# Kernel tuning notes

Hardware: AMD Instinct MI355X
Metric: run time of the kernel (lower is better)

The kernel has to match this reference:

```python
import jax, jax.numpy as jnp
import numpy as np

H, P, G, NS, K = 8, 64, 64, 64, 3          # heads, dim_head, slice_num, d_state, d_conv
D_INNER = H * P                            # 512
CONV_DIM = D_INNER + 2 * NS                # 640
D_IN_PROJ = 2 * D_INNER + 2 * NS + 2 * H   # 1168


def setup_inputs() -> dict:
    key = jax.random.key(0)
    ks = jax.random.split(key, 10)
    dim, Bsz, N = 256, 4, 8192
    s = 0.02
    return {
        "x": jax.random.normal(ks[0], (Bsz, N, dim), jnp.float32),
        "W_fx": jax.random.normal(ks[1], (D_INNER, dim), jnp.float32) * s,
        "b_fx": jnp.zeros((D_INNER,), jnp.float32),
        "W_x": jax.random.normal(ks[2], (D_INNER, dim), jnp.float32) * s,
        "b_x": jnp.zeros((D_INNER,), jnp.float32),
        "W_slice": jax.random.normal(ks[3], (G, P), jnp.float32) * s,
        "b_slice": jnp.zeros((G,), jnp.float32),
        "temperature": jnp.full((1, H, 1, 1), 0.5, jnp.float32),
        "hy_in_w": jax.random.normal(ks[4], (D_IN_PROJ, D_INNER), jnp.float32) * s,
        "hy_conv_w": jax.random.normal(ks[5], (CONV_DIM, K), jnp.float32) * s,
        "hy_conv_b": jnp.zeros((CONV_DIM,), jnp.float32),
        "hy_dt_bias": jnp.log(jnp.expm1(jnp.full((H,), 0.01, jnp.float32))),
        "hy_A_log": jnp.log(jnp.linspace(1.0, 16.0, H)).astype(jnp.float32),
        "hy_D": jnp.ones((H,), jnp.float32),
        "hy_fcD_w": jax.random.normal(ks[6], (H, D_INNER), jnp.float32) * s,
        "hy_norm_w": jnp.ones((D_INNER,), jnp.float32),
        "hy_out_w": jax.random.normal(ks[7], (D_INNER, D_INNER), jnp.float32) * s,
        "out_w": jax.random.normal(ks[8], (dim, D_INNER), jnp.float32) * s,
        "out_b": jnp.zeros((dim,), jnp.float32),
    }


def _hydra(u, in_w, conv_w, conv_b, dt_bias, A_log, Dp, fcD_w, norm_w, out_w):
    # Bidirectional Mamba2-style selective scan (Hydra, non mem-eff path).
    Bt, L, _ = u.shape
    zxbcdt = u @ in_w.T                                   # (B, L, 1168)
    z = zxbcdt[..., :D_INNER]
    xBC = zxbcdt[..., D_INNER:D_INNER + CONV_DIM]
    dt = zxbcdt[..., -2 * H:]
    # fwd dts for fwd copies, time-flipped bwd dts stacked along batch
    dt = jnp.concatenate([dt[..., :H], jnp.flip(dt[..., H:], axis=1)], axis=0)
    dt = jax.nn.softplus(dt + dt_bias)                    # (2B, L, H)
    # depthwise causal conv, kernel K, left pad K-1 then silu
    xp = jnp.pad(xBC, ((0, 0), (K - 1, 0), (0, 0)))
    xBC = sum(xp[:, k:k + L, :] * conv_w[:, k] for k in range(K)) + conv_b
    xBC = jax.nn.silu(xBC)
    x = xBC[..., :D_INNER]
    Bm = xBC[..., D_INNER:D_INNER + NS]
    Cm = xBC[..., D_INNER + NS:]
    x_og = x
    x2 = jnp.concatenate([x, jnp.flip(x, 1)], 0).reshape(2 * Bt, L, H, P)
    B2 = jnp.concatenate([Bm, jnp.flip(Bm, 1)], 0)        # (2B, L, NS)
    C2 = jnp.concatenate([Cm, jnp.flip(Cm, 1)], 0)
    dA = jnp.exp(dt * (-jnp.exp(A_log)))                  # (2B, L, H)
    dBx = jnp.einsum('blh,bln,blhp->blhpn', dt, B2, x2)   # (2B, L, H, P, NS)

    def step(h, inp):
        dA_t, dBx_t, C_t = inp
        h = h * dA_t[:, :, None, None] + dBx_t
        return h, jnp.einsum('bhpn,bn->bhp', h, C_t)

    h0 = jnp.zeros((2 * Bt, H, P, NS), u.dtype)
    _, ys = jax.lax.scan(step, h0, (dA.transpose(1, 0, 2), dBx.transpose(1, 0, 2, 3, 4), C2.transpose(1, 0, 2)))
    y = ys.transpose(1, 0, 2, 3).reshape(2 * Bt, L, D_INNER)
    y_fw, y_bw = y[:Bt], jnp.flip(y[Bt:], 1)
    # quasiseparable: strictly-lower (shift fwd) + strictly-upper (shift bwd) + diagonal
    y = jnp.pad(y_fw[:, :-1], ((0, 0), (1, 0), (0, 0))) + jnp.pad(y_bw[:, 1:], ((0, 0), (0, 1), (0, 0)))
    y = y + x_og * jnp.repeat(x_og @ fcD_w.T + Dp, P, axis=-1)
    # gated RMSNorm (gate before norm), then out projection
    yg = y * jax.nn.silu(z)
    yg = yg * jax.lax.rsqrt(jnp.mean(jnp.square(yg), -1, keepdims=True) + 1e-5) * norm_w
    return yg @ out_w.T


def reference(x, W_fx, b_fx, W_x, b_x, W_slice, b_slice, temperature,
              hy_in_w, hy_conv_w, hy_conv_b, hy_dt_bias, hy_A_log, hy_D,
              hy_fcD_w, hy_norm_w, hy_out_w, out_w, out_b):
    B, N, _ = x.shape
    fx = (x @ W_fx.T + b_fx).reshape(B, N, H, P).transpose(0, 2, 1, 3)   # (B,H,N,P)
    xm = (x @ W_x.T + b_x).reshape(B, N, H, P).transpose(0, 2, 1, 3)
    temp = jnp.maximum(temperature, 1e-6)
    sw = jax.nn.softmax((xm @ W_slice.T + b_slice) / temp, axis=-1)      # (B,H,N,G)
    snorm = sw.sum(2)                                                     # (B,H,G)
    st = jnp.einsum('bhnc,bhng->bhgc', fx, sw) / (snorm + 1e-5)[..., None]
    st = st.transpose(0, 2, 1, 3).reshape(B, G, D_INNER)                  # (B,G,512)
    ot = _hydra(st, hy_in_w, hy_conv_w, hy_conv_b, hy_dt_bias, hy_A_log, hy_D,
                hy_fcD_w, hy_norm_w, hy_out_w)
    ot = ot.reshape(B, G, H, P).transpose(0, 2, 1, 3)                     # (B,H,G,P)
    out = jnp.einsum('bhgc,bhng->bhnc', ot, sw).transpose(0, 2, 1, 3).reshape(B, N, D_INNER)
    return out @ out_w.T + out_b
```

## Files before the change

### kernel.cpp

```cpp
#include <hip/hip_runtime.h>
#include <hip/hip_bf16.h>
#include <cstdint>
#include <cstddef>

#define Hh 8
#define DIN 512
#define CONVD 640
#define DPROJ 1168
#define NTOK 8192
#define DIM 256

typedef __attribute__((ext_vector_type(8))) short short8;
typedef __attribute__((ext_vector_type(4))) float f32x4;

static __device__ __forceinline__ float sigmoidf_(float x) { return 1.f / (1.f + expf(-x)); }
static __device__ __forceinline__ unsigned short f2b(float f) {
  __hip_bfloat16 h = __float2bfloat16(f);
  return *(unsigned short*)&h;
}
static __device__ __forceinline__ float b2f(unsigned short u) {
  union { unsigned int i; float f; } cv; cv.i = ((unsigned int)u) << 16; return cv.f;
}
static __device__ __forceinline__ void gll16(const void* g, void* l) {
  __builtin_amdgcn_global_load_lds((const __attribute__((address_space(1))) void*)g,
                                   (__attribute__((address_space(3))) void*)l, 16, 0, 0);
}

__global__ __launch_bounds__(256) void k_cvt(
    const float* __restrict__ wfx, const float* __restrict__ wx, const float* __restrict__ outw,
    const float* __restrict__ inw, const float* __restrict__ how,
    const float* __restrict__ bfx, const float* __restrict__ bx,
    unsigned short* __restrict__ wcat, unsigned short* __restrict__ outwb,
    unsigned short* __restrict__ inwb, unsigned short* __restrict__ howb,
    float* __restrict__ bcat) {
  const int e = (blockIdx.x * 256 + threadIdx.x) * 4;
  if (e >= 1253376) {
    const int i = e - 1253376;
    float4 v;
    if (i < 512) v = *(const float4*)(bfx + i);
    else         v = *(const float4*)(bx + (i - 512));
    *(float4*)(bcat + i) = v;
    return;
  }
  const float* src; unsigned short* dst; int i;
  if (e < 131072)        { i = e;           src = wfx;  dst = wcat; }
  else if (e < 262144)   { i = e - 131072;  src = wx;   dst = wcat + 131072; }
  else if (e < 393216)   { i = e - 262144;  src = outw; dst = outwb; }
  else if (e < 991232)   { i = e - 393216;  src = inw;  dst = inwb; }
  else                   { i = e - 991232;  src = how;  dst = howb; }
  float4 v = *(const float4*)(src + i);
  ushort4 o;
  o.x = f2b(v.x); o.y = f2b(v.y); o.z = f2b(v.z); o.w = f2b(v.w);
  *(ushort4*)(dst + i) = o;
}

__global__ __launch_bounds__(256) void k_cvtx(
    const float* __restrict__ x, unsigned short* __restrict__ xb) {
  const int e = (blockIdx.x * 256 + threadIdx.x) * 8;
  float4 v0 = *(const float4*)(x + e);
  float4 v1 = *(const float4*)(x + e + 4);
  short8 o;
  o[0] = (short)f2b(v0.x); o[1] = (short)f2b(v0.y);
  o[2] = (short)f2b(v0.z); o[3] = (short)f2b(v0.w);
  o[4] = (short)f2b(v1.x); o[5] = (short)f2b(v1.y);
  o[6] = (short)f2b(v1.z); o[7] = (short)f2b(v1.w);
  *(short8*)(xb + e) = o;
}

__global__ __launch_bounds__(256) void k_front(
    const unsigned short* __restrict__ xb, const unsigned short* __restrict__ wcat,
    const float* __restrict__ bcat, const float* __restrict__ Wslice,
    const float* __restrict__ bslice, const float* __restrict__ temperature,
    unsigned short* __restrict__ cb, unsigned short* __restrict__ swb) {
  __shared__ unsigned short lds[32768];
  const int tid = threadIdx.x;
  const int m0 = blockIdx.x * 128;
  const int n0 = blockIdx.y * 128;
  const int w = tid >> 6, lane = tid & 63;
  const int l15 = lane & 15, kq = lane >> 4;
  const int wm = (w & 1) * 64, wn = (w >> 1) * 64;
  float bs[4];
#pragma unroll
  for (int j = 0; j < 4; ++j) bs[j] = bcat[n0 + wn + j * 16 + l15];
  f32x4 acc[4][4];
#pragma unroll
  for (int i = 0; i < 4; ++i)
#pragma unroll
    for (int j = 0; j < 4; ++j) acc[i][j] = (f32x4){0.f, 0.f, 0.f, 0.f};

  auto stage = [&](int buf, int kt) {
    unsigned short* As = lds + buf * 8192;
    unsigned short* Bs = lds + 16384 + buf * 8192;
#pragma unroll
    for (int i = 0; i < 4; ++i) {
      const int c = tid + 256 * i;
      const int m = c >> 3, kb = c & 7;
      const int kbs = (kb ^ (m & 7)) * 8;
      gll16(&xb[(size_t)(m0 + m) * 256 + kt + kbs], &As[c * 8]);
      gll16(&wcat[(size_t)(n0 + m) * 256 + kt + kbs], &Bs[c * 8]);
    }
  };

  stage(0, 0);
  __syncthreads();
  int buf = 0;
  for (int t = 0; t < 4; ++t) {
    if (t < 3) stage(buf ^ 1, (t + 1) * 64);
    const unsigned short* As = lds + buf * 8192;
    const unsigned short* Bs = lds + 16384 + buf * 8192;
#pragma unroll
    for (int kw = 0; kw < 2; ++kw) {
      short8 af[4], bfr[4];
#pragma unroll
      for (int i = 0; i < 4; ++i) {
        const int rm = wm + i * 16 + l15;
        af[i]  = *(const short8*)&As[rm * 64 + ((kw * 32 + kq * 8) ^ ((rm & 7) << 3))];
        const int rn = wn + i * 16 + l15;
        bfr[i] = *(const short8*)&Bs[rn * 64 + ((kw * 32 + kq * 8) ^ ((rn & 7) << 3))];
      }
#pragma unroll
      for (int i = 0; i < 4; ++i)
#pragma unroll
        for (int j = 0; j < 4; ++j)
          acc[i][j] = __builtin_amdgcn_mfma_f32_16x16x32_bf16(af[i], bfr[j], acc[i][j], 0, 0, 0);
    }
    __syncthreads();
    buf ^= 1;
  }
  unsigned short* Cs = lds;
#pragma unroll
  for (int i = 0; i < 4; ++i)
#pragma unroll
    for (int j = 0; j < 4; ++j)
#pragma unroll
      for (int r = 0; r < 4; ++r) {
        const int m = wm + i * 16 + kq * 4 + r;
        const int n = wn + j * 16 + l15;
        Cs[m * 136 + n] = f2b(acc[i][j][r] + bs[j]);
      }
  __syncthreads();
  if (blockIdx.y < 4) {
#pragma unroll
    for (int it = 0; it < 8; ++it) {
      const int c = tid + 256 * it;
      const int m = c >> 4, seg = c & 15;
      *(short8*)&cb[(size_t)(m0 + m) * 512 + n0 + seg * 8] = *(const short8*)&Cs[m * 136 + seg * 8];
    }
    return;
  }
  const int h0 = (n0 - 512) >> 6;
  const int bidx = m0 >> 13, nb = m0 & (NTOK - 1);
  short8 sbfr[2][4];
#pragma unroll
  for (int kt = 0; kt < 2; ++kt)
#pragma unroll
    for (int j = 0; j < 4; ++j) {
      const float* wp = Wslice + (j * 16 + l15) * 64 + kt * 32 + kq * 8;
      short8 t;
#pragma unroll
      for (int u = 0; u < 8; ++u) t[u] = (short)f2b(wp[u]);
      sbfr[kt][j] = t;
    }
  float sbs[4];
#pragma unroll
  for (int j = 0; j < 4; ++j) sbs[j] = bslice[j * 16 + l15];
  f32x4 sacc[2][2][4];
#pragma unroll
  for (int hl = 0; hl < 2; ++hl)
#pragma unroll
    for (int i = 0; i < 2; ++i)
#pragma unroll
      for (int j = 0; j < 4; ++j) sacc[hl][i][j] = (f32x4){0.f, 0.f, 0.f, 0.f};
#pragma unroll
  for (int hl = 0; hl < 2; ++hl)
#pragma unroll
    for (int kt = 0; kt < 2; ++kt) {
      short8 af[2];
#pragma unroll
      for (int i = 0; i < 2; ++i)
        af[i] = *(const short8*)&Cs[(w * 32 + i * 16 + l15) * 136 + hl * 64 + kt * 32 + kq * 8];
#pragma unroll
      for (int i = 0; i < 2; ++i)
#pragma unroll
        for (int j = 0; j < 4; ++j)
          sacc[hl][i][j] = __builtin_amdgcn_mfma_f32_16x16x32_bf16(af[i], sbfr[kt][j], sacc[hl][i][j], 0, 0, 0);
    }
  __syncthreads();
#pragma unroll
  for (int hl = 0; hl < 2; ++hl) {
    const float invt = 1.f / fmaxf(temperature[h0 + hl], 1e-6f);
#pragma unroll
    for (int i = 0; i < 2; ++i)
#pragma unroll
      for (int r = 0; r < 4; ++r) {
        float v[4];
        float m = -1e30f;
#pragma unroll
        for (int j = 0; j < 4; ++j) { v[j] = (sacc[hl][i][j][r] + sbs[j]) * invt; m = fmaxf(m, v[j]); }
#pragma unroll
        for (int off = 8; off; off >>= 1) m = fmaxf(m, __shfl_xor(m, off));
        float s = 0.f;
#pragma unroll
        for (int j = 0; j < 4; ++j) { v[j] = expf(v[j] - m); s += v[j]; }
#pragma unroll
        for (int off = 8; off; off >>= 1) s += __shfl_xor(s, off);
        const float inv = 1.f / s;
        const int row = w * 32 + i * 16 + kq * 4 + r;
#pragma unroll
        for (int j = 0; j < 4; ++j) Cs[row * 136 + hl * 64 + j * 16 + l15] = f2b(v[j] * inv);
      }
  }
  __syncthreads();
#pragma unroll
  for (int it = 0; it < 8; ++it) {
    const int c = tid + 256 * it;
    const int head = c >> 10, row = (c >> 3) & 127, seg = c & 7;
    *(short8*)&swb[((size_t)(bidx * 8 + h0 + head) * NTOK + nb + row) * 64 + seg * 8] =
        *(const short8*)&Cs[row * 136 + head * 64 + seg * 8];
  }
}

__global__ __launch_bounds__(256) void k_st(
    const unsigned short* __restrict__ swb, const unsigned short* __restrict__ cb,
    float* __restrict__ st_raw, float* __restrict__ snorm) {
  __shared__ unsigned short swT[64][136];
  __shared__ unsigned short fxT[64][136];
  const int tid = threadIdx.x;
  const int bh = blockIdx.y;
  const int b = bh >> 3, h = bh & 7;
  const int nbase = blockIdx.x * 512;
  const int w = tid >> 6, lane = tid & 63;
  const int l15 = lane & 15, kq = lane >> 4;
  f32x4 acc[4];
#pragma unroll
  for (int i = 0; i < 4; ++i) acc[i] = (f32x4){0.f, 0.f, 0.f, 0.f};
  float sn = 0.f;
  for (int nc = 0; nc < 4; ++nc) {
    const int n0 = nbase + nc * 128;
#pragma unroll
    for (int i = 0; i < 4; ++i) {
      const int c = tid + 256 * i, n = c >> 3, gc = c & 7;
      short8 sv = *(const short8*)&swb[((size_t)bh * NTOK + n0 + n) * 64 + gc * 8];
      short8 fv = *(const short8*)&cb[((size_t)(b * NTOK) + n0 + n) * 512 + h * 64 + gc * 8];
#pragma unroll
      for (int u = 0; u < 8; ++u) {
        swT[gc * 8 + u][n] = (unsigned short)sv[u];
        fxT[gc * 8 + u][n] = (unsigned short)fv[u];
      }
    }
    __syncthreads();
    {
      const int g = tid & 63, q = tid >> 6;
#pragma unroll
      for (int nn = 0; nn < 32; ++nn) sn += b2f(swT[g][q * 32 + nn]);
    }
#pragma unroll
    for (int kw = 0; kw < 4; ++kw) {
      short8 bfr = *(const short8*)&fxT[w * 16 + l15][kw * 32 + kq * 8];
#pragma unroll
      for (int mi = 0; mi < 4; ++mi) {
        short8 af = *(const short8*)&swT[mi * 16 + l15][kw * 32 + kq * 8];
        acc[mi] = __builtin_amdgcn_mfma_f32_16x16x32_bf16(af, bfr, acc[mi], 0, 0, 0);
      }
    }
    __syncthreads();
  }
  float* stp = st_raw + (size_t)bh * 4096;
#pragma unroll
  for (int mi = 0; mi < 4; ++mi)
#pragma unroll
    for (int r = 0; r < 4; ++r)
      atomicAdd(&stp[(mi * 16 + kq * 4 + r) * 64 + w * 16 + l15], acc[mi][r]);
  atomicAdd(&snorm[bh * 64 + (tid & 63)], sn);
}

__global__ __launch_bounds__(256) void k_stnorm(
    const float* __restrict__ st_raw, const float* __restrict__ snorm,
    unsigned short* __restrict__ st2b) {
  const int idx = blockIdx.x * 256 + threadIdx.x;
  const int p = idx & 63, g = (idx >> 6) & 63, h = (idx >> 12) & 7, b = idx >> 15;
  const float v = st_raw[idx] / (snorm[(b * Hh + h) * 64 + g] + 1e-5f);
  st2b[(size_t)(b * 64 + g) * DIN + h * 64 + p] = f2b(v);
}

__global__ __launch_bounds__(256) void k_inproj(
    const unsigned short* __restrict__ st2b, const unsigned short* __restrict__ inwb,
    float* __restrict__ zx) {
  const int tid = threadIdx.x;
  const int m0 = blockIdx.x * 64;
  const int n0 = blockIdx.y * 64;
  const int w = tid >> 6, lane = tid & 63;
  const int l15 = lane & 15, kq = lane >> 4;
  f32x4 acc[4];
#pragma unroll
  for (int j = 0; j < 4; ++j) acc[j] = (f32x4){0.f, 0.f, 0.f, 0.f};
  const int arow = m0 + w * 16 + l15;
#pragma unroll
  for (int kc = 0; kc < 16; ++kc) {
    const short8 af = *(const short8*)&st2b[(size_t)arow * DIN + kc * 32 + kq * 8];
#pragma unroll
    for (int j = 0; j < 4; ++j) {
      int brow = n0 + j * 16 + l15;
      if (brow >= DPROJ) brow = 0;
      const short8 bfr = *(const short8*)&inwb[(size_t)brow * DIN + kc * 32 + kq * 8];
      acc[j] = __builtin_amdgcn_mfma_f32_16x16x32_bf16(af, bfr, acc[j], 0, 0, 0);
    }
  }
#pragma unroll
  for (int j = 0; j < 4; ++j)
#pragma unroll
    for (int r = 0; r < 4; ++r) {
      const int m = m0 + w * 16 + kq * 4 + r;
      const int c = n0 + j * 16 + l15;
      if (c < DPROJ) zx[(size_t)m * DPROJ + c] = acc[j][r];
    }
}

__global__ __launch_bounds__(256) void k_prep(
    const float* __restrict__ zx, const float* __restrict__ convw, const float* __restrict__ convb,
    const float* __restrict__ dtbias, const float* __restrict__ Alog,
    float* __restrict__ xbc, float* __restrict__ dt2, float* __restrict__ ldA2) {
  const int idx = blockIdx.x * 256 + threadIdx.x;
  const int NCONV = 4 * 64 * CONVD;
  if (idx < NCONV) {
    const int c = idx % CONVD;
    const int l = (idx / CONVD) & 63;
    const int b = idx / (CONVD * 64);
    float acc = convb[c];
#pragma unroll
    for (int k = 0; k < 3; ++k) {
      const int ls = l - 2 + k;
      if (ls >= 0) acc += zx[(size_t)(b * 64 + ls) * DPROJ + DIN + c] * convw[c * 3 + k];
    }
    xbc[idx] = acc * sigmoidf_(acc);
  } else if (idx < NCONV + 8 * 64 * 8) {
    const int j = idx - NCONV;
    const int h = j & 7, l = (j >> 3) & 63, bb = j >> 9;
    float raw;
    if (bb < 4) raw = zx[(size_t)(bb * 64 + l) * DPROJ + 1152 + h];
    else        raw = zx[(size_t)((bb - 4) * 64 + (63 - l)) * DPROJ + 1160 + h];
    const float d = raw + dtbias[h];
    const float sp = (d > 20.f) ? d : log1pf(expf(d));
    dt2[j] = sp;
    ldA2[j] = sp * -expf(Alog[h]);
  }
}

__global__ __launch_bounds__(256) void k_ssm(
    const float* __restrict__ xbc, const float* __restrict__ dt2, const float* __restrict__ ldA2,
    float* __restrict__ ys) {
  __shared__ unsigned short s_C[64][72];
  __shared__ unsigned short s_Bm[64][72];
  __shared__ unsigned short s_X[64][72];
  __shared__ unsigned short s_G[64][72];
  __shared__ float s_L[64];
  __shared__ float s_dt[64];
  const int blk = blockIdx.x;
  const int h = blk & 7, bb = blk >> 3;
  const int b = (bb < 4) ? bb : bb - 4;
  const bool rev = bb >= 4;
  const int tid = threadIdx.x;
  const int w = tid >> 6, lane = tid & 63;
  const int l15 = lane & 15, kq = lane >> 4;
  {
    const int l = tid >> 2, part = tid & 3;
    const int t = rev ? 63 - l : l;
    const float* src = xbc + (size_t)(b * 64 + l) * CONVD + DIN + part * 32;
#pragma unroll
    for (int u = 0; u < 32; u += 4) {
      float4 v = *(const float4*)(src + u);
      const int c = part * 32 + u;
      unsigned short* dst = (c < 64) ? &s_Bm[t][c] : &s_C[t][c - 64];
      dst[0] = f2b(v.x); dst[1] = f2b(v.y); dst[2] = f2b(v.z); dst[3] = f2b(v.w);
    }
    const float* xs = xbc + (size_t)(b * 64 + l) * CONVD + h * 64 + part * 16;
#pragma unroll
    for (int u = 0; u < 16; u += 4) {
      float4 v = *(const float4*)(xs + u);
      const int p = part * 16 + u;
      s_X[p + 0][t] = f2b(v.x); s_X[p + 1][t] = f2b(v.y);
      s_X[p + 2][t] = f2b(v.z); s_X[p + 3][t] = f2b(v.w);
    }
  }
  if (w == 0) {
    const float dtv = dt2[(bb * 64 + lane) * 8 + h];
    float ld = ldA2[(bb * 64 + lane) * 8 + h];
#pragma unroll
    for (int off = 1; off < 64; off <<= 1) {
      const float o = __shfl_up(ld, off);
      if (lane >= off) ld += o;
    }
    s_L[lane] = ld;
    s_dt[lane] = dtv;
  }
  __syncthreads();
  f32x4 accS[4];
#pragma unroll
  for (int i = 0; i < 4; ++i) accS[i] = (f32x4){0.f, 0.f, 0.f, 0.f};
#pragma unroll
  for (int kw = 0; kw < 2; ++kw) {
    const short8 bfr = *(const short8*)&s_Bm[w * 16 + l15][kw * 32 + kq * 8];
#pragma unroll
    for (int i = 0; i < 4; ++i) {
      const short8 af = *(const short8*)&s_C[i * 16 + l15][kw * 32 + kq * 8];
      accS[i] = __builtin_amdgcn_mfma_f32_16x16x32_bf16(af, bfr, accS[i], 0, 0, 0);
    }
  }
  const int s_idx = w * 16 + l15;
  const float Ls = s_L[s_idx];
  const float dts = s_dt[s_idx];
#pragma unroll
  for (int i = 0; i < 4; ++i)
#pragma unroll
    for (int r = 0; r < 4; ++r) {
      const int t = i * 16 + kq * 4 + r;
      const float g = (s_idx <= t) ? accS[i][r] * expf(s_L[t] - Ls) * dts : 0.f;
      s_G[t][s_idx] = f2b(g);
    }
  __syncthreads();
  f32x4 accY[4];
#pragma unroll
  for (int i = 0; i < 4; ++i) accY[i] = (f32x4){0.f, 0.f, 0.f, 0.f};
#pragma unroll
  for (int kw = 0; kw < 2; ++kw) {
    const short8 bfr = *(const short8*)&s_X[w * 16 + l15][kw * 32 + kq * 8];
#pragma unroll
    for (int i = 0; i < 4; ++i) {
      const short8 af = *(const short8*)&s_G[i * 16 + l15][kw * 32 + kq * 8];
      accY[i] = __builtin_amdgcn_mfma_f32_16x16x32_bf16(af, bfr, accY[i], 0, 0, 0);
    }
  }
#pragma unroll
  for (int i = 0; i < 4; ++i)
#pragma unroll
    for (int r = 0; r < 4; ++r) {
      const int t = i * 16 + kq * 4 + r;
      ys[(((size_t)(bb * 64 + t) * 8 + h) << 6) + w * 16 + l15] = accY[i][r];
    }
}

__global__ __launch_bounds__(256) void k_gate(
    const float* __restrict__ ys, const float* __restrict__ xbc, const float* __restrict__ zx,
    const float* __restrict__ fcdw, const float* __restrict__ Dp,
    const float* __restrict__ normw, unsigned short* __restrict__ ygb) {
  __shared__ float red[256][9];
  __shared__ float s_xfc[8];
  const int bl = blockIdx.x;
  const int b = bl >> 6, l = bl & 63;
  const int tid = threadIdx.x;
  const float xog0 = xbc[(size_t)bl * CONVD + tid];
  const float xog1 = xbc[(size_t)bl * CONVD + 256 + tid];
#pragma unroll
  for (int h = 0; h < 8; ++h)
    red[tid][h] = xog0 * fcdw[h * DIN + tid] + xog1 * fcdw[h * DIN + 256 + tid];
  __syncthreads();
  for (int s = 128; s > 0; s >>= 1) {
    if (tid < s) {
#pragma unroll
      for (int h = 0; h < 8; ++h) red[tid][h] += red[tid + s][h];
    }
    __syncthreads();
  }
  if (tid < 8) s_xfc[tid] = red[0][tid] + Dp[tid];
  __syncthreads();
  float ygv[2];
  float sumsq = 0.f;
#pragma unroll
  for (int ci = 0; ci < 2; ++ci) {
    const int c = tid + ci * 256;
    const int h = c >> 6, p = c & 63;
    float yv = 0.f;
    if (l >= 1)  yv += ys[(((size_t)(b * 64 + (l - 1)) * 8 + h) << 6) + p];
    if (l <= 62) yv += ys[(((size_t)((4 + b) * 64 + (62 - l)) * 8 + h) << 6) + p];
    const float xog = (ci == 0) ? xog0 : xog1;
    yv += xog * s_xfc[h];
    const float z = zx[(size_t)bl * DPROJ + c];
    const float g = yv * (z * sigmoidf_(z));
    ygv[ci] = g;
    sumsq += g * g;
  }
  red[tid][0] = sumsq;
  __syncthreads();
  for (int s = 128; s > 0; s >>= 1) {
    if (tid < s) red[tid][0] += red[tid + s][0];
    __syncthreads();
  }
  const float scale = 1.f / sqrtf(red[0][0] / 512.f + 1e-5f);
#pragma unroll
  for (int ci = 0; ci < 2; ++ci) {
    const int c = tid + ci * 256;
    ygb[(size_t)bl * DIN + c] = f2b(ygv[ci] * scale * normw[c]);
  }
}

__global__ __launch_bounds__(256) void k_oproj(
    const unsigned short* __restrict__ ygb, const unsigned short* __restrict__ howb,
    unsigned short* __restrict__ otT) {
  __shared__ unsigned short Cs[64][72];
  const int tid = threadIdx.x;
  const int b = blockIdx.x;
  const int h = blockIdx.y;
  const int m0 = b * 64, n0 = h * 64;
  const int w = tid >> 6, lane = tid & 63;
  const int l15 = lane & 15, kq = lane >> 4;
  f32x4 acc[4];
#pragma unroll
  for (int j = 0; j < 4; ++j) acc[j] = (f32x4){0.f, 0.f, 0.f, 0.f};
  const int arow = m0 + w * 16 + l15;
#pragma unroll
  for (int kc = 0; kc < 16; ++kc) {
    const short8 af = *(const short8*)&ygb[(size_t)arow * DIN + kc * 32 + kq * 8];
#pragma unroll
    for (int j = 0; j < 4; ++j) {
      const int brow = n0 + j * 16 + l15;
      const short8 bfr = *(const short8*)&howb[(size_t)brow * DIN + kc * 32 + kq * 8];
      acc[j] = __builtin_amdgcn_mfma_f32_16x16x32_bf16(af, bfr, acc[j], 0, 0, 0);
    }
  }
#pragma unroll
  for (int j = 0; j < 4; ++j)
#pragma unroll
    for (int r = 0; r < 4; ++r) {
      const int g = w * 16 + kq * 4 + r;
      const int p = j * 16 + l15;
      Cs[p][g] = f2b(acc[j][r]);
    }
  __syncthreads();
#pragma unroll
  for (int it = 0; it < 2; ++it) {
    const int c = tid + 256 * it;
    const int p = c >> 3, seg = c & 7;
    *(short8*)&otT[(((size_t)(b * 8 + h) * 64 + p) << 6) + seg * 8] = *(const short8*)&Cs[p][seg * 8];
  }
}

__global__ __launch_bounds__(256) void k_mixfinal(
    const unsigned short* __restrict__ swb, const unsigned short* __restrict__ otT,
    const unsigned short* __restrict__ outwb, const float* __restrict__ outb,
    float* __restrict__ out) {
  __shared__ unsigned short lm[33280];
  const int blk = blockIdx.x;
  const int b = blk >> 7;
  const int t0 = (blk & 127) * 64;
  const int tid = threadIdx.x;
  const int w = tid >> 6, lane = tid & 63;
  const int l15 = lane & 15, kq = lane >> 4;
#pragma unroll
  for (int hh = 0; hh < 2; ++hh) {
    const int h = w * 2 + hh;
    const int bh = b * 8 + h;
    f32x4 acc[4][4];
#pragma unroll
    for (int i = 0; i < 4; ++i)
#pragma unroll
      for (int j = 0; j < 4; ++j) acc[i][j] = (f32x4){0.f, 0.f, 0.f, 0.f};
#pragma unroll
    for (int kt = 0; kt < 2; ++kt) {
      short8 af[4], bfr[4];
#pragma unroll
      for (int i = 0; i < 4; ++i) {
        af[i]  = *(const short8*)&swb[((size_t)bh * NTOK + t0 + i * 16 + l15) * 64 + kt * 32 + kq * 8];
        bfr[i] = *(const short8*)&otT[(((size_t)bh * 64 + i * 16 + l15) << 6) + kt * 32 + kq * 8];
      }
#pragma unroll
      for (int i = 0; i < 4; ++i)
#pragma unroll
        for (int j = 0; j < 4; ++j)
          acc[i][j] = __builtin_amdgcn_mfma_f32_16x16x32_bf16(af[i], bfr[j], acc[i][j], 0, 0, 0);
    }
#pragma unroll
    for (int i = 0; i < 4; ++i)
#pragma unroll
      for (int j = 0; j < 4; ++j)
#pragma unroll
        for (int r = 0; r < 4; ++r)
          lm[(i * 16 + kq * 4 + r) * 520 + h * 64 + j * 16 + l15] = f2b(acc[i][j][r]);
  }
  __syncthreads();
  float ob[4];
#pragma unroll
  for (int j = 0; j < 4; ++j) ob[j] = outb[w * 64 + j * 16 + l15];
  f32x4 facc[4][4];
#pragma unroll
  for (int i = 0; i < 4; ++i)
#pragma unroll
    for (int j = 0; j < 4; ++j) facc[i][j] = (f32x4){0.f, 0.f, 0.f, 0.f};
#pragma unroll
  for (int kt = 0; kt < 16; ++kt) {
    short8 af[4], bfr[4];
#pragma unroll
    for (int i = 0; i < 4; ++i) {
      af[i]  = *(const short8*)&lm[(i * 16 + l15) * 520 + kt * 32 + kq * 8];
      bfr[i] = *(const short8*)&outwb[(size_t)(w * 64 + i * 16 + l15) * 512 + kt * 32 + kq * 8];
    }
#pragma unroll
    for (int i = 0; i < 4; ++i)
#pragma unroll
      for (int j = 0; j < 4; ++j)
        facc[i][j] = __builtin_amdgcn_mfma_f32_16x16x32_bf16(af[i], bfr[j], facc[i][j], 0, 0, 0);
  }
  __syncthreads();
  float* lf = (float*)lm;
#pragma unroll
  for (int i = 0; i < 4; ++i)
#pragma unroll
    for (int j = 0; j < 4; ++j)
#pragma unroll
      for (int r = 0; r < 4; ++r)
        lf[(i * 16 + kq * 4 + r) * 260 + w * 64 + j * 16 + l15] = facc[i][j][r] + ob[j];
  __syncthreads();
#pragma unroll
  for (int it = 0; it < 16; ++it) {
    const int c = tid + 256 * it;
    const int row = c >> 6, seg = c & 63;
    *(float4*)&out[((size_t)(b * NTOK + t0 + row)) * 256 + seg * 4] =
        *(const float4*)&lf[row * 260 + seg * 4];
  }
}

extern "C" void kernel_launch(void* const* d_in, const int* in_sizes, int n_in,
                              void* d_out, int out_size, void* d_ws, size_t ws_size,
                              hipStream_t stream) {
  const float* x      = (const float*)d_in[0];
  const float* Wfx    = (const float*)d_in[1];
  const float* bfx    = (const float*)d_in[2];
  const float* Wx     = (const float*)d_in[3];
  const float* bx     = (const float*)d_in[4];
  const float* Wslice = (const float*)d_in[5];
  const float* bslice = (const float*)d_in[6];
  const float* temp   = (const float*)d_in[7];
  const float* inw    = (const float*)d_in[8];
  const float* convw  = (const float*)d_in[9];
  const float* convb  = (const float*)d_in[10];
  const float* dtbias = (const float*)d_in[11];
  const float* Alog   = (const float*)d_in[12];
  const float* Dp     = (const float*)d_in[13];
  const float* fcdw   = (const float*)d_in[14];
  const float* normw  = (const float*)d_in[15];
  const float* how    = (const float*)d_in[16];
  const float* outw   = (const float*)d_in[17];
  const float* outb   = (const float*)d_in[18];

  unsigned short* us = (unsigned short*)d_ws;
  unsigned short* cb     = us;
  unsigned short* swb    = cb + 16777216;
  unsigned short* wcatb  = swb + 16777216;
  unsigned short* outwbf = wcatb + 262144;
  unsigned short* otTb   = outwbf + 131072;
  unsigned short* inwb   = otTb + 131072;
  unsigned short* howb   = inwb + 598016;
  unsigned short* st2b   = howb + 262144;
  unsigned short* ygbb   = st2b + 131072;
  unsigned short* xbb    = ygbb + 131072;
  float* fbase = (float*)(xbb + 8388608);
  float* bcat   = fbase;
  float* st_raw = bcat + 1024;
  float* snorm  = st_raw + 131072;
  float* zx     = snorm + 2048;
  float* xbc    = zx + 299008;
  float* dt2    = xbc + 163840;
  float* ldA2   = dt2 + 4096;
  float* ysb    = ldA2 + 4096;

  hipMemsetAsync(st_raw, 0, (131072 + 2048) * sizeof(float), stream);

  k_cvt     <<<dim3(1225),    256, 0, stream>>>(Wfx, Wx, outw, inw, how, bfx, bx,
                                                wcatb, outwbf, inwb, howb, bcat);
  k_cvtx    <<<dim3(4096),    256, 0, stream>>>(x, xbb);
  k_front   <<<dim3(256, 8),  256, 0, stream>>>(xbb, wcatb, bcat, Wslice, bslice, temp, cb, swb);
  k_st      <<<dim3(16, 32),  256, 0, stream>>>(swb, cb, st_raw, snorm);
  k_stnorm  <<<dim3(512),     256, 0, stream>>>(st_raw, snorm, st2b);
  k_inproj  <<<dim3(4, 19),   256, 0, stream>>>(st2b, inwb, zx);
  k_prep    <<<dim3(656),     256, 0, stream>>>(zx, convw, convb, dtbias, Alog, xbc, dt2, ldA2);
  k_ssm     <<<dim3(64),      256, 0, stream>>>(xbc, dt2, ldA2, ysb);
  k_gate    <<<dim3(256),     256, 0, stream>>>(ysb, xbc, zx, fcdw, Dp, normw, ygbb);
  k_oproj   <<<dim3(4, 8),    256, 0, stream>>>(ygbb, howb, otTb);
  k_mixfinal<<<dim3(512),     256, 0, stream>>>(swb, otTb, outwbf, outb, (float*)d_out);
}
```

Measured before the change: 258.1 us.

## Replace atomics with partial buffers, compute slice norms via MFMA, swizzle LDS, merge convert kernels

Merges the x conversion into the weight conversion kernel, removing one launch and the memset. k_st now writes per-block partial sums instead of using atomicAdd, and k_stnorm reduces the 16 partials. The slice-weight column sums are computed with an extra MFMA against a vector of ones instead of a scalar LDS loop. The transposed LDS writes use an XOR swizzle to cut bank conflicts. The cost is extra partial-buffer traffic and more reads in k_stnorm.

Result: faster. 249.9 us (-3.2%).

```diff
diff --git a/kernel.cpp b/kernel.cpp
--- a/kernel.cpp
+++ b/kernel.cpp
@@ -30,10 +30,24 @@
     const float* __restrict__ wfx, const float* __restrict__ wx, const float* __restrict__ outw,
     const float* __restrict__ inw, const float* __restrict__ how,
     const float* __restrict__ bfx, const float* __restrict__ bx,
+    const float* __restrict__ x,
     unsigned short* __restrict__ wcat, unsigned short* __restrict__ outwb,
     unsigned short* __restrict__ inwb, unsigned short* __restrict__ howb,
-    float* __restrict__ bcat) {
-  const int e = (blockIdx.x * 256 + threadIdx.x) * 4;
+    float* __restrict__ bcat, unsigned short* __restrict__ xb) {
+  const int blk = blockIdx.x;
+  if (blk < 4096) {
+    const int e = (blk * 256 + threadIdx.x) * 8;
+    float4 v0 = *(const float4*)(x + e);
+    float4 v1 = *(const float4*)(x + e + 4);
+    short8 o;
+    o[0] = (short)f2b(v0.x); o[1] = (short)f2b(v0.y);
+    o[2] = (short)f2b(v0.z); o[3] = (short)f2b(v0.w);
+    o[4] = (short)f2b(v1.x); o[5] = (short)f2b(v1.y);
+    o[6] = (short)f2b(v1.z); o[7] = (short)f2b(v1.w);
+    *(short8*)(xb + e) = o;
+    return;
+  }
+  const int e = ((blk - 4096) * 256 + threadIdx.x) * 4;
   if (e >= 1253376) {
     const int i = e - 1253376;
     float4 v;
@@ -52,19 +66,6 @@
   ushort4 o;
   o.x = f2b(v.x); o.y = f2b(v.y); o.z = f2b(v.z); o.w = f2b(v.w);
   *(ushort4*)(dst + i) = o;
-}
-
-__global__ __launch_bounds__(256) void k_cvtx(
-    const float* __restrict__ x, unsigned short* __restrict__ xb) {
-  const int e = (blockIdx.x * 256 + threadIdx.x) * 8;
-  float4 v0 = *(const float4*)(x + e);
-  float4 v1 = *(const float4*)(x + e + 4);
-  short8 o;
-  o[0] = (short)f2b(v0.x); o[1] = (short)f2b(v0.y);
-  o[2] = (short)f2b(v0.z); o[3] = (short)f2b(v0.w);
-  o[4] = (short)f2b(v1.x); o[5] = (short)f2b(v1.y);
-  o[6] = (short)f2b(v1.z); o[7] = (short)f2b(v1.w);
-  *(short8*)(xb + e) = o;
 }
 
 __global__ __launch_bounds__(256) void k_front(
@@ -222,7 +223,7 @@
 
 __global__ __launch_bounds__(256) void k_st(
     const unsigned short* __restrict__ swb, const unsigned short* __restrict__ cb,
-    float* __restrict__ st_raw, float* __restrict__ snorm) {
+    float* __restrict__ st_part, float* __restrict__ sn_part) {
   __shared__ unsigned short swT[64][136];
   __shared__ unsigned short fxT[64][136];
   const int tid = threadIdx.x;
@@ -231,10 +232,15 @@
   const int nbase = blockIdx.x * 512;
   const int w = tid >> 6, lane = tid & 63;
   const int l15 = lane & 15, kq = lane >> 4;
-  f32x4 acc[4];
-#pragma unroll
-  for (int i = 0; i < 4; ++i) acc[i] = (f32x4){0.f, 0.f, 0.f, 0.f};
-  float sn = 0.f;
+  short8 ones;
+#pragma unroll
+  for (int u = 0; u < 8; ++u) ones[u] = (short)0x3F80;
+  f32x4 acc[4], accO[4];
+#pragma unroll
+  for (int i = 0; i < 4; ++i) {
+    acc[i] = (f32x4){0.f, 0.f, 0.f, 0.f};
+    accO[i] = (f32x4){0.f, 0.f, 0.f, 0.f};
+  }
   for (int nc = 0; nc < 4; ++nc) {
     const int n0 = nbase + nc * 128;
 #pragma unroll
@@ -242,44 +248,59 @@
       const int c = tid + 256 * i, n = c >> 3, gc = c & 7;
       short8 sv = *(const short8*)&swb[((size_t)bh * NTOK + n0 + n) * 64 + gc * 8];
       short8 fv = *(const short8*)&cb[((size_t)(b * NTOK) + n0 + n) * 512 + h * 64 + gc * 8];
+      const int csw = n ^ (gc << 4);
 #pragma unroll
       for (int u = 0; u < 8; ++u) {
-        swT[gc * 8 + u][n] = (unsigned short)sv[u];
-        fxT[gc * 8 + u][n] = (unsigned short)fv[u];
+        swT[gc * 8 + u][csw] = (unsigned short)sv[u];
+        fxT[gc * 8 + u][csw] = (unsigned short)fv[u];
       }
     }
     __syncthreads();
-    {
-      const int g = tid & 63, q = tid >> 6;
-#pragma unroll
-      for (int nn = 0; nn < 32; ++nn) sn += b2f(swT[g][q * 32 + nn]);
-    }
 #pragma unroll
     for (int kw = 0; kw < 4; ++kw) {
-      short8 bfr = *(const short8*)&fxT[w * 16 + l15][kw * 32 + kq * 8];
+      const int brow = w * 16 + l15;
+      const short8 bfr = *(const short8*)&fxT[brow][(kw * 32 + kq * 8) ^ ((brow >> 3) << 4)];
 #pragma unroll
       for (int mi = 0; mi < 4; ++mi) {
-        short8 af = *(const short8*)&swT[mi * 16 + l15][kw * 32 + kq * 8];
+        const int arow = mi * 16 + l15;
+        const short8 af = *(const short8*)&swT[arow][(kw * 32 + kq * 8) ^ ((arow >> 3) << 4)];
         acc[mi] = __builtin_amdgcn_mfma_f32_16x16x32_bf16(af, bfr, acc[mi], 0, 0, 0);
+        if (w == 0)
+          accO[mi] = __builtin_amdgcn_mfma_f32_16x16x32_bf16(af, ones, accO[mi], 0, 0, 0);
       }
     }
     __syncthreads();
   }
-  float* stp = st_raw + (size_t)bh * 4096;
+  float* stp = st_part + ((size_t)blockIdx.x * 32 + bh) * 4096;
 #pragma unroll
   for (int mi = 0; mi < 4; ++mi)
 #pragma unroll
     for (int r = 0; r < 4; ++r)
-      atomicAdd(&stp[(mi * 16 + kq * 4 + r) * 64 + w * 16 + l15], acc[mi][r]);
-  atomicAdd(&snorm[bh * 64 + (tid & 63)], sn);
+      stp[(mi * 16 + kq * 4 + r) * 64 + w * 16 + l15] = acc[mi][r];
+  if (w == 0 && l15 == 0) {
+    float* snp = sn_part + ((size_t)blockIdx.x * 32 + bh) * 64;
+#pragma unroll
+    for (int mi = 0; mi < 4; ++mi)
+#pragma unroll
+      for (int r = 0; r < 4; ++r)
+        snp[mi * 16 + kq * 4 + r] = accO[mi][r];
+  }
 }
 
 __global__ __launch_bounds__(256) void k_stnorm(
-    const float* __restrict__ st_raw, const float* __restrict__ snorm,
+    const float* __restrict__ st_part, const float* __restrict__ sn_part,
     unsigned short* __restrict__ st2b) {
   const int idx = blockIdx.x * 256 + threadIdx.x;
   const int p = idx & 63, g = (idx >> 6) & 63, h = (idx >> 12) & 7, b = idx >> 15;
-  const float v = st_raw[idx] / (snorm[(b * Hh + h) * 64 + g] + 1e-5f);
+  const int bh = idx >> 12;
+  const int gp = idx & 4095;
+  float s = 0.f, sn = 0.f;
+#pragma unroll
+  for (int bx = 0; bx < 16; ++bx) {
+    s  += st_part[((size_t)bx * 32 + bh) * 4096 + gp];
+    sn += sn_part[((size_t)bx * 32 + bh) * 64 + g];
+  }
+  const float v = s / (sn + 1e-5f);
   st2b[(size_t)(b * 64 + g) * DIN + h * 64 + p] = f2b(v);
 }
 
@@ -653,23 +674,20 @@
   unsigned short* ygbb   = st2b + 131072;
   unsigned short* xbb    = ygbb + 131072;
   float* fbase = (float*)(xbb + 8388608);
-  float* bcat   = fbase;
-  float* st_raw = bcat + 1024;
-  float* snorm  = st_raw + 131072;
-  float* zx     = snorm + 2048;
-  float* xbc    = zx + 299008;
-  float* dt2    = xbc + 163840;
-  float* ldA2   = dt2 + 4096;
-  float* ysb    = ldA2 + 4096;
-
-  hipMemsetAsync(st_raw, 0, (131072 + 2048) * sizeof(float), stream);
-
-  k_cvt     <<<dim3(1225),    256, 0, stream>>>(Wfx, Wx, outw, inw, how, bfx, bx,
-                                                wcatb, outwbf, inwb, howb, bcat);
-  k_cvtx    <<<dim3(4096),    256, 0, stream>>>(x, xbb);
+  float* bcat    = fbase;
+  float* st_part = bcat + 1024;
+  float* sn_part = st_part + 2097152;
+  float* zx      = sn_part + 32768;
+  float* xbc     = zx + 299008;
+  float* dt2     = xbc + 163840;
+  float* ldA2    = dt2 + 4096;
+  float* ysb     = ldA2 + 4096;
+
+  k_cvt     <<<dim3(5321),    256, 0, stream>>>(Wfx, Wx, outw, inw, how, bfx, bx, x,
+                                                wcatb, outwbf, inwb, howb, bcat, xbb);
   k_front   <<<dim3(256, 8),  256, 0, stream>>>(xbb, wcatb, bcat, Wslice, bslice, temp, cb, swb);
-  k_st      <<<dim3(16, 32),  256, 0, stream>>>(swb, cb, st_raw, snorm);
-  k_stnorm  <<<dim3(512),     256, 0, stream>>>(st_raw, snorm, st2b);
+  k_st      <<<dim3(16, 32),  256, 0, stream>>>(swb, cb, st_part, sn_part);
+  k_stnorm  <<<dim3(512),     256, 0, stream>>>(st_part, sn_part, st2b);
   k_inproj  <<<dim3(4, 19),   256, 0, stream>>>(st2b, inwb, zx);
   k_prep    <<<dim3(656),     256, 0, stream>>>(zx, convw, convb, dtbias, Alog, xbc, dt2, ldA2);
   k_ssm     <<<dim3(64),      256, 0, stream>>>(xbc, dt2, ldA2, ysb);
```
